# Performance work log

Hardware: AMD Instinct MI355X
Metric: run time of the kernel (lower is better)

Reference implementation:

```python
import jax, jax.numpy as jnp
import numpy as np

D_MODEL = 1024
NUM_HEADS = 16
HEAD_DIM = D_MODEL // NUM_HEADS
BATCH = 2
SEQ = 2048


def setup_inputs() -> dict:
    key = jax.random.key(0)
    ks = jax.random.split(key, 9)
    s_in = 1.0 / np.sqrt(D_MODEL)  # kaiming-ish fan-in scaling for stability
    return {
        "x": jax.random.normal(ks[0], (BATCH, SEQ, D_MODEL), jnp.float32),
        "wq": jax.random.normal(ks[1], (D_MODEL, D_MODEL), jnp.float32) * s_in,
        "bq": jnp.zeros((D_MODEL,), jnp.float32),
        "wk": jax.random.normal(ks[2], (D_MODEL, D_MODEL), jnp.float32) * s_in,
        "bk": jnp.zeros((D_MODEL,), jnp.float32),
        "wv": jax.random.normal(ks[3], (D_MODEL, D_MODEL), jnp.float32) * s_in,
        "bv": jnp.zeros((D_MODEL,), jnp.float32),
        "wo": jax.random.normal(ks[4], (D_MODEL, D_MODEL), jnp.float32) * s_in,
        "bo": jnp.zeros((D_MODEL,), jnp.float32),
    }


def reference(x, wq, bq, wk, bk, wv, bv, wo, bo):
    B, S, _ = x.shape
    # QKV projections, split heads: [B, H, S, Dh]
    def proj(w, b):
        y = x @ w + b
        return y.reshape(B, S, NUM_HEADS, HEAD_DIM).transpose(0, 2, 1, 3)

    q = proj(wq, bq)
    k = proj(wk, bk)
    v = proj(wv, bv)

    scale = 1.0 / jnp.sqrt(jnp.float32(HEAD_DIM))
    scores = jnp.einsum("bhsd,bhtd->bhst", q, k) * scale  # [B,H,S,S]
    attn = jax.nn.softmax(scores, axis=-1)
    out = jnp.einsum("bhst,bhtd->bhsd", attn, v)  # [B,H,S,Dh]
    out = out.transpose(0, 2, 1, 3).reshape(B, S, D_MODEL)
    return out @ wo + bo
```

## Files before the change

kernel.cpp:

```cpp
#include <hip/hip_runtime.h>
#include <stdint.h>
#include <stddef.h>


typedef __attribute__((ext_vector_type(8))) short short8;
typedef __attribute__((ext_vector_type(4))) float f32x4;
typedef __attribute__((ext_vector_type(16))) float f32x16;
typedef __attribute__((ext_vector_type(4))) unsigned short u16x4;

#define MFMA16(a, b, c) __builtin_amdgcn_mfma_f32_16x16x32_bf16((a), (b), (c), 0, 0, 0)
#define MFMA32(a, b, c) __builtin_amdgcn_mfma_f32_32x32x16_bf16((a), (b), (c), 0, 0, 0)
#define AS1 __attribute__((address_space(1)))
#define AS3 __attribute__((address_space(3)))

__device__ __forceinline__ unsigned short f2bf(float f) {
  union { float f; unsigned u; } v; v.f = f;
  unsigned r = v.u + 0x7fffu + ((v.u >> 16) & 1u);
  return (unsigned short)(r >> 16);
}

__device__ __forceinline__ float fexp2(float x) {
#if __has_builtin(__builtin_amdgcn_exp2f)
  return __builtin_amdgcn_exp2f(x);
#else
  return __builtin_exp2f(x);
#endif
}

__device__ __forceinline__ unsigned cvt_pk_bf16(float lo, float hi) {
  unsigned r;
  asm("v_cvt_pk_bf16_f32 %0, %1, %2" : "=v"(r) : "v"(lo), "v"(hi));
  return r;
}

__device__ __forceinline__ void pl32_swap(unsigned& a, unsigned& b) {
  asm volatile("v_permlane32_swap_b32 %0, %1" : "+v"(a), "+v"(b));
}

__device__ __forceinline__ short8 mk8(unsigned a, unsigned b, unsigned c, unsigned d) {
  union { unsigned u[4]; short8 s; } v;
  v.u[0] = a; v.u[1] = b; v.u[2] = c; v.u[3] = d;
  return v.s;
}

__global__ __launch_bounds__(256) void prep_all_kernel(const float* __restrict__ x,
                                                       const float* __restrict__ wq,
                                                       const float* __restrict__ wk,
                                                       const float* __restrict__ wv,
                                                       const float* __restrict__ wo,
                                                       const float* __restrict__ bq,
                                                       const float* __restrict__ bk,
                                                       const float* __restrict__ bv,
                                                       unsigned short* __restrict__ xb,
                                                       unsigned short* __restrict__ wt,
                                                       float* __restrict__ bias3) {
  __shared__ unsigned short t_lds[32][33];
  const int bid = blockIdx.x;
  if (bid < 4096) {
    int wsel = bid >> 10;
    int rem = bid & 1023;
    int kb = (rem >> 5) << 5;
    int nb = (rem & 31) << 5;
    const float* W = (wsel == 0) ? wq : (wsel == 1) ? wk : (wsel == 2) ? wv : wo;
    int t = threadIdx.x;
    int r = t >> 3, c = (t & 7) * 4;
    float4 v = *reinterpret_cast<const float4*>(W + (size_t)(kb + r) * 1024 + nb + c);
    t_lds[r][c + 0] = f2bf(v.x);
    t_lds[r][c + 1] = f2bf(v.y);
    t_lds[r][c + 2] = f2bf(v.z);
    t_lds[r][c + 3] = f2bf(v.w);
    __syncthreads();
    u16x4 o;
    o.x = t_lds[c + 0][r]; o.y = t_lds[c + 1][r];
    o.z = t_lds[c + 2][r]; o.w = t_lds[c + 3][r];
    *reinterpret_cast<u16x4*>(wt + (size_t)(wsel * 1024 + nb + r) * 1024 + kb + c) = o;
  } else if (bid < 8192) {
    int i = ((bid - 4096) * 256 + threadIdx.x) * 4;
    float4 v = *reinterpret_cast<const float4*>(x + i);
    u16x4 o;
    o.x = f2bf(v.x); o.y = f2bf(v.y); o.z = f2bf(v.z); o.w = f2bf(v.w);
    *reinterpret_cast<u16x4*>(xb + i) = o;
  } else {
#pragma unroll
    for (int k = 0; k < 12; ++k) {
      int i = k * 256 + threadIdx.x;
      bias3[i] = (i < 1024) ? bq[i] : (i < 2048) ? bk[i - 1024] : bv[i - 2048];
    }
  }
}

template <typename OutT, bool QS>
__global__ __launch_bounds__(256) void gemm_bt_kernel(const unsigned short* __restrict__ A,
                                                      const unsigned short* __restrict__ Bt,
                                                      const float* __restrict__ bias,
                                                      OutT* __restrict__ C, int N) {
  constexpr int K = 1024;
  __shared__ __align__(16) unsigned short a_lds[2][128 * 32];
  __shared__ __align__(16) unsigned short b_lds[2][128 * 32];
  const int nb = N >> 7;
  const int nwg = nb << 5;
  const int cpx = nwg >> 3;
  const int wg = ((int)blockIdx.x & 7) * cpx + ((int)blockIdx.x >> 3);
  const int bm = wg / nb;
  const int bn = wg % nb;
  const int m0 = bm << 7, n0 = bn << 7;
  const int tid = threadIdx.x;
  const int w = tid >> 6, l = tid & 63;
  const int lr = l & 15, lg = l >> 4;
  const int wm = (w >> 1) << 6, wn = (w & 1) << 6;

  const int q0 = w * 2, q1 = w * 2 + 1;
  const unsigned short* pa0 = A + (size_t)(m0 + q0 * 16 + (l >> 2)) * K + (l & 3) * 8;
  const unsigned short* pa1 = A + (size_t)(m0 + q1 * 16 + (l >> 2)) * K + (l & 3) * 8;
  const unsigned short* pb0 = Bt + (size_t)(n0 + q0 * 16 + (l >> 2)) * K + (l & 3) * 8;
  const unsigned short* pb1 = Bt + (size_t)(n0 + q1 * 16 + (l >> 2)) * K + (l & 3) * 8;

#define GEMM_STAGE(buf, k0)                                                        \
  do {                                                                             \
    __builtin_amdgcn_global_load_lds((const AS1 void*)(pa0 + (k0)),                \
        (AS3 void*)(&a_lds[buf][q0 * 512]), 16, 0, 0);                             \
    __builtin_amdgcn_global_load_lds((const AS1 void*)(pa1 + (k0)),                \
        (AS3 void*)(&a_lds[buf][q1 * 512]), 16, 0, 0);                             \
    __builtin_amdgcn_global_load_lds((const AS1 void*)(pb0 + (k0)),                \
        (AS3 void*)(&b_lds[buf][q0 * 512]), 16, 0, 0);                             \
    __builtin_amdgcn_global_load_lds((const AS1 void*)(pb1 + (k0)),                \
        (AS3 void*)(&b_lds[buf][q1 * 512]), 16, 0, 0);                             \
  } while (0)

  f32x4 acc[4][4] = {};
  GEMM_STAGE(0, 0);
  __syncthreads();

  int cur = 0;
  for (int k0 = 0; k0 < K; k0 += 32) {
    if (k0 + 32 < K) GEMM_STAGE(cur ^ 1, k0 + 32);
    short8 af[4], bfr[4];
#pragma unroll
    for (int i = 0; i < 4; ++i)
      af[i] = *reinterpret_cast<const short8*>(&a_lds[cur][(wm + i * 16 + lr) * 32 + lg * 8]);
#pragma unroll
    for (int i = 0; i < 4; ++i)
      bfr[i] = *reinterpret_cast<const short8*>(&b_lds[cur][(wn + i * 16 + lr) * 32 + lg * 8]);
#pragma unroll
    for (int i = 0; i < 4; ++i)
#pragma unroll
      for (int j = 0; j < 4; ++j)
        acc[i][j] = MFMA16(af[i], bfr[j], acc[i][j]);
    __syncthreads();
    cur ^= 1;
  }
#undef GEMM_STAGE

  const float scale = (QS && n0 < 1024) ? 0.18033688011111f : 1.0f;
#pragma unroll
  for (int i = 0; i < 4; ++i) {
#pragma unroll
    for (int j = 0; j < 4; ++j) {
#pragma unroll
      for (int r = 0; r < 4; ++r) {
        int m = m0 + wm + i * 16 + lg * 4 + r;
        int n = n0 + wn + j * 16 + lr;
        float val = (acc[i][j][r] + bias[n]) * scale;
        if constexpr (sizeof(OutT) == 2) {
          C[(size_t)m * N + n] = (OutT)f2bf(val);
        } else {
          C[(size_t)m * N + n] = val;
        }
      }
    }
  }
}

__device__ __forceinline__ void stage_v(char* vw, int pi, int vd0, short8 va, short8 vb) {
  union { short8 s; unsigned u[4]; } ua, ub;
  ua.s = va; ub.s = vb;
#pragma unroll
  for (int jr = 0; jr < 4; ++jr) {
    unsigned w0 = __builtin_amdgcn_perm(ub.u[jr], ua.u[jr], 0x05040100u);
    unsigned w1 = __builtin_amdgcn_perm(ub.u[jr], ua.u[jr], 0x07060302u);
    int d0 = vd0 + 2 * jr, d1 = d0 + 1;
    *reinterpret_cast<unsigned*>(vw + d0 * 128 + ((4 * pi) ^ ((d0 & 7) << 4))) = w0;
    *reinterpret_cast<unsigned*>(vw + d1 * 128 + ((4 * pi) ^ ((d1 & 7) << 4))) = w1;
  }
}

__global__ __launch_bounds__(512, 4) void attn_kernel(const unsigned short* __restrict__ qkv,
                                                       unsigned short* __restrict__ aout) {
  __shared__ __align__(16) char lds[65536];
  const int tid = threadIdx.x;
  const int w = tid >> 6, l = tid & 63;
  const int kv = w >> 2, wsub = w & 3;
  const int lq = l & 31;
  const int hi = l >> 5;
  const int wg = ((int)blockIdx.x & 7) * 64 + ((int)blockIdx.x >> 3);
  const int bh = wg >> 4, qblk = wg & 15;
  const int b = bh >> 4, h = bh & 15;
  const size_t rowbase = (size_t)b * 2048;
  const int q0 = qblk * 128 + wsub * 32;
  const int base = kv << 15;

  short8 qf[4];
  {
    const unsigned short* qrow = qkv + (rowbase + q0 + lq) * 3072 + h * 64 + hi * 8;
#pragma unroll
    for (int c = 0; c < 4; ++c)
      qf[c] = *reinterpret_cast<const short8*>(qrow + c * 16);
  }

  const int colsw = (16 * (l & 7)) ^ ((l >> 3) << 4);
  const char* ksrc = (const char*)(qkv + (rowbase + kv * 1024) * 3072 + 1024 + h * 64) +
                     (size_t)(16 * wsub + (l >> 3)) * 6144 + colsw;
  const int kdst = wsub * 2048;

  const int pi = tid & 31;
  const int vd0 = ((tid >> 5) & 7) * 8;
  const unsigned short* vbase = qkv + (rowbase + kv * 1024) * 3072 + 2048 + h * 64;
  const int swz_lq = (lq & 7) << 4;

  short8 ones;
  {
    union { unsigned u[4]; short8 s; } o_;
    o_.u[0] = o_.u[1] = o_.u[2] = o_.u[3] = 0x3F803F80u;
    ones = o_.s;
  }

  f32x16 ot0 = {}, ot1 = {}, lacc = {};

  __builtin_amdgcn_global_load_lds((const AS1 void*)ksrc,
                                   (AS3 void*)(lds + base + kdst), 16, 0, 0);
  __builtin_amdgcn_global_load_lds((const AS1 void*)(ksrc + 49152),
                                   (AS3 void*)(lds + base + kdst + 1024), 16, 0, 0);
  ksrc += 393216;
  {
    short8 va = *reinterpret_cast<const short8*>(vbase + (size_t)(2 * pi) * 3072 + vd0);
    short8 vb = *reinterpret_cast<const short8*>(vbase + (size_t)(2 * pi + 1) * 3072 + vd0);
    stage_v(lds + base + 16384, pi, vd0, va, vb);
  }

  int cur = 0;
  for (int t0 = 0; t0 < 1024; t0 += 64) {
    __syncthreads();
    const bool more = (t0 + 64) < 1024;
    short8 vna, vnb;
    if (more) {
      char* kd = lds + base + ((cur ^ 1) << 13) + kdst;
      __builtin_amdgcn_global_load_lds((const AS1 void*)ksrc, (AS3 void*)kd, 16, 0, 0);
      __builtin_amdgcn_global_load_lds((const AS1 void*)(ksrc + 49152),
                                       (AS3 void*)(kd + 1024), 16, 0, 0);
      ksrc += 393216;
      vna = *reinterpret_cast<const short8*>(vbase + (size_t)(t0 + 64 + 2 * pi) * 3072 + vd0);
      vnb = *reinterpret_cast<const short8*>(vbase + (size_t)(t0 + 65 + 2 * pi) * 3072 + vd0);
    }
    const char* kl = lds + base + (cur << 13);
    const char* vl = lds + base + 16384 + (cur << 13);

    f32x16 s0 = {}, s1 = {};
    __builtin_amdgcn_s_setprio(1);
#pragma unroll
    for (int c = 0; c < 4; ++c) {
      short8 kf0 = *reinterpret_cast<const short8*>(kl + lq * 128 + ((c * 32 + hi * 16) ^ swz_lq));
      short8 kf1 = *reinterpret_cast<const short8*>(kl + (32 + lq) * 128 + ((c * 32 + hi * 16) ^ swz_lq));
      s0 = MFMA32(kf0, qf[c], s0);
      s1 = MFMA32(kf1, qf[c], s1);
    }
    __builtin_amdgcn_s_setprio(0);

    if (more) stage_v(lds + base + 16384 + ((cur ^ 1) << 13), pi, vd0, vna, vnb);

#pragma unroll
    for (int c = 0; c < 4; ++c) {
      float t0_, t1_, t2_, t3_, t4_, t5_, t6_, t7_;
      if (c < 2) {
        const int o = c * 8;
        t0_ = fexp2(s0[o + 0]); t1_ = fexp2(s0[o + 1]);
        t2_ = fexp2(s0[o + 2]); t3_ = fexp2(s0[o + 3]);
        t4_ = fexp2(s0[o + 4]); t5_ = fexp2(s0[o + 5]);
        t6_ = fexp2(s0[o + 6]); t7_ = fexp2(s0[o + 7]);
      } else {
        const int o = (c - 2) * 8;
        t0_ = fexp2(s1[o + 0]); t1_ = fexp2(s1[o + 1]);
        t2_ = fexp2(s1[o + 2]); t3_ = fexp2(s1[o + 3]);
        t4_ = fexp2(s1[o + 4]); t5_ = fexp2(s1[o + 5]);
        t6_ = fexp2(s1[o + 6]); t7_ = fexp2(s1[o + 7]);
      }
      unsigned a0 = cvt_pk_bf16(t0_, t1_), a1 = cvt_pk_bf16(t4_, t5_);
      unsigned b0 = cvt_pk_bf16(t2_, t3_), b1 = cvt_pk_bf16(t6_, t7_);
      pl32_swap(a0, a1); pl32_swap(b0, b1);
      short8 pfc = mk8(a0, b0, a1, b1);
      short8 vf0 = *reinterpret_cast<const short8*>(vl + lq * 128 + ((c * 32 + hi * 16) ^ swz_lq));
      short8 vf1 = *reinterpret_cast<const short8*>(vl + (32 + lq) * 128 + ((c * 32 + hi * 16) ^ swz_lq));
      __builtin_amdgcn_s_setprio(1);
      ot0 = MFMA32(vf0, pfc, ot0);
      ot1 = MFMA32(vf1, pfc, ot1);
      lacc = MFMA32(ones, pfc, lacc);
      __builtin_amdgcn_s_setprio(0);
    }
    cur ^= 1;
  }

  __syncthreads();
  float* lbuf = (float*)lds;
  if (kv == 1) {
    float* ob = (float*)(lds + 32768 + wsub * 8192);
#pragma unroll
    for (int r = 0; r < 16; ++r) {
      int d = (r & 3) + 8 * (r >> 2) + 4 * hi;
      ob[d * 32 + lq] = ot0[r];
      ob[(32 + d) * 32 + lq] = ot1[r];
    }
    if (hi == 0) lbuf[wsub * 32 + lq] = lacc[0];
  }
  __syncthreads();
  if (kv == 0) {
    const float* ob = (const float*)(lds + 32768 + wsub * 8192);
    const float inv = 1.0f / (lacc[0] + lbuf[wsub * 32 + lq]);
    char* st = lds + 8192;
    const int qq = wsub * 32 + lq;
    const int swz = (qq & 7) << 4;
#pragma unroll
    for (int r = 0; r < 16; r += 2) {
      int d = (r & 3) + 8 * (r >> 2) + 4 * hi;
      float a0 = (ot0[r] + ob[d * 32 + lq]) * inv;
      float a1 = (ot0[r + 1] + ob[(d + 1) * 32 + lq]) * inv;
      *(unsigned*)(st + qq * 128 + ((2 * d) ^ swz)) = cvt_pk_bf16(a0, a1);
      float b0_ = (ot1[r] + ob[(32 + d) * 32 + lq]) * inv;
      float b1_ = (ot1[r + 1] + ob[(33 + d) * 32 + lq]) * inv;
      *(unsigned*)(st + qq * 128 + ((2 * (32 + d)) ^ swz)) = cvt_pk_bf16(b0_, b1_);
    }
  }
  __syncthreads();
  {
    int row = tid >> 2;
    int c2 = (tid & 3) * 2;
    int swzr = (row & 7) << 4;
    const char* src = lds + 8192 + row * 128;
    short8 v0 = *reinterpret_cast<const short8*>(src + ((c2 * 16) ^ swzr));
    short8 v1 = *reinterpret_cast<const short8*>(src + (((c2 + 1) * 16) ^ swzr));
    unsigned short* orow = aout + (rowbase + qblk * 128 + row) * 1024 + h * 64 + c2 * 8;
    *reinterpret_cast<short8*>(orow) = v0;
    *reinterpret_cast<short8*>(orow + 8) = v1;
  }
}

extern "C" void kernel_launch(void* const* d_in, const int* in_sizes, int n_in,
                              void* d_out, int out_size, void* d_ws, size_t ws_size,
                              hipStream_t stream) {
  const float* x  = (const float*)d_in[0];
  const float* wq = (const float*)d_in[1];
  const float* bq = (const float*)d_in[2];
  const float* wk = (const float*)d_in[3];
  const float* bk = (const float*)d_in[4];
  const float* wv = (const float*)d_in[5];
  const float* bv = (const float*)d_in[6];
  const float* wo = (const float*)d_in[7];
  const float* bo = (const float*)d_in[8];
  float* out = (float*)d_out;

  char* ws = (char*)d_ws;
  unsigned short* xb    = (unsigned short*)(ws);
  unsigned short* aob   = (unsigned short*)(ws);
  unsigned short* wt    = (unsigned short*)(ws + 8388608);
  float*          bias3 = (float*)(ws + 16777216);
  unsigned short* qkvb  = (unsigned short*)(ws + 16842752);

  prep_all_kernel<<<8193, 256, 0, stream>>>(x, wq, wk, wv, wo, bq, bk, bv, xb, wt, bias3);

  gemm_bt_kernel<unsigned short, true><<<768, 256, 0, stream>>>(xb, wt, bias3, qkvb, 3072);

  attn_kernel<<<512, 512, 0, stream>>>(qkvb, aob);

  gemm_bt_kernel<float, false><<<256, 256, 0, stream>>>(aob, wt + (size_t)3072 * 1024, bo, out, 1024);
}
```

Measured before the change: 116.0 us.

## Pre-transpose V in a separate kernel and stream it via async LDS loads

Adds a kernel that writes V in per-head transposed [d][t] layout to workspace. The attention kernel then loads V tiles with global_load_lds, the same way it loads K, instead of register loads followed by perm-based LDS staging. This drops per-iteration VGPR traffic and the perm work inside the attention loop. In exchange it adds a kernel launch and an extra round trip of V (about 8 MB) through global memory.

```diff
diff --git a/kernel.cpp b/kernel.cpp
--- a/kernel.cpp
+++ b/kernel.cpp
@@ -89,6 +89,29 @@
   }
 }
 
+__global__ __launch_bounds__(256) void vt_kernel(const unsigned short* __restrict__ qkv,
+                                                 unsigned short* __restrict__ vt) {
+  __shared__ unsigned short t_lds[32][33];
+  const int bid = blockIdx.x;
+  const int T0 = (bid >> 5) << 5;
+  const int D0 = (bid & 31) << 5;
+  const int t = threadIdx.x;
+  const int r = t >> 3, c = (t & 7) * 4;
+  u16x4 v = *reinterpret_cast<const u16x4*>(qkv + (size_t)(T0 + r) * 3072 + 2048 + D0 + c);
+  t_lds[r][c + 0] = v.x;
+  t_lds[r][c + 1] = v.y;
+  t_lds[r][c + 2] = v.z;
+  t_lds[r][c + 3] = v.w;
+  __syncthreads();
+  u16x4 o;
+  o.x = t_lds[c + 0][r]; o.y = t_lds[c + 1][r];
+  o.z = t_lds[c + 2][r]; o.w = t_lds[c + 3][r];
+  const int d = D0 + r;
+  const int b = T0 >> 11, h = d >> 6, dloc = d & 63;
+  *reinterpret_cast<u16x4*>(vt + (size_t)(b * 16 + h) * 131072 + (size_t)dloc * 2048 +
+                            (T0 & 2047) + c) = o;
+}
+
 template <typename OutT, bool QS>
 __global__ __launch_bounds__(256) void gemm_bt_kernel(const unsigned short* __restrict__ A,
                                                       const unsigned short* __restrict__ Bt,
@@ -171,21 +194,9 @@
   }
 }
 
-__device__ __forceinline__ void stage_v(char* vw, int pi, int vd0, short8 va, short8 vb) {
-  union { short8 s; unsigned u[4]; } ua, ub;
-  ua.s = va; ub.s = vb;
-#pragma unroll
-  for (int jr = 0; jr < 4; ++jr) {
-    unsigned w0 = __builtin_amdgcn_perm(ub.u[jr], ua.u[jr], 0x05040100u);
-    unsigned w1 = __builtin_amdgcn_perm(ub.u[jr], ua.u[jr], 0x07060302u);
-    int d0 = vd0 + 2 * jr, d1 = d0 + 1;
-    *reinterpret_cast<unsigned*>(vw + d0 * 128 + ((4 * pi) ^ ((d0 & 7) << 4))) = w0;
-    *reinterpret_cast<unsigned*>(vw + d1 * 128 + ((4 * pi) ^ ((d1 & 7) << 4))) = w1;
-  }
-}
-
 __global__ __launch_bounds__(512, 4) void attn_kernel(const unsigned short* __restrict__ qkv,
-                                                       unsigned short* __restrict__ aout) {
+                                                      const unsigned short* __restrict__ vt,
+                                                      unsigned short* __restrict__ aout) {
   __shared__ __align__(16) char lds[65536];
   const int tid = threadIdx.x;
   const int w = tid >> 6, l = tid & 63;
@@ -210,11 +221,10 @@
   const int colsw = (16 * (l & 7)) ^ ((l >> 3) << 4);
   const char* ksrc = (const char*)(qkv + (rowbase + kv * 1024) * 3072 + 1024 + h * 64) +
                      (size_t)(16 * wsub + (l >> 3)) * 6144 + colsw;
+  const char* vsrc = (const char*)vt + (size_t)bh * 262144 +
+                     (size_t)(16 * wsub + (l >> 3)) * 4096 + kv * 2048 + colsw;
   const int kdst = wsub * 2048;
 
-  const int pi = tid & 31;
-  const int vd0 = ((tid >> 5) & 7) * 8;
-  const unsigned short* vbase = qkv + (rowbase + kv * 1024) * 3072 + 2048 + h * 64;
   const int swz_lq = (lq & 7) << 4;
 
   short8 ones;
@@ -230,26 +240,28 @@
                                    (AS3 void*)(lds + base + kdst), 16, 0, 0);
   __builtin_amdgcn_global_load_lds((const AS1 void*)(ksrc + 49152),
                                    (AS3 void*)(lds + base + kdst + 1024), 16, 0, 0);
+  __builtin_amdgcn_global_load_lds((const AS1 void*)vsrc,
+                                   (AS3 void*)(lds + base + 16384 + kdst), 16, 0, 0);
+  __builtin_amdgcn_global_load_lds((const AS1 void*)(vsrc + 32768),
+                                   (AS3 void*)(lds + base + 16384 + kdst + 1024), 16, 0, 0);
   ksrc += 393216;
-  {
-    short8 va = *reinterpret_cast<const short8*>(vbase + (size_t)(2 * pi) * 3072 + vd0);
-    short8 vb = *reinterpret_cast<const short8*>(vbase + (size_t)(2 * pi + 1) * 3072 + vd0);
-    stage_v(lds + base + 16384, pi, vd0, va, vb);
-  }
+  vsrc += 128;
 
   int cur = 0;
   for (int t0 = 0; t0 < 1024; t0 += 64) {
     __syncthreads();
     const bool more = (t0 + 64) < 1024;
-    short8 vna, vnb;
     if (more) {
       char* kd = lds + base + ((cur ^ 1) << 13) + kdst;
       __builtin_amdgcn_global_load_lds((const AS1 void*)ksrc, (AS3 void*)kd, 16, 0, 0);
       __builtin_amdgcn_global_load_lds((const AS1 void*)(ksrc + 49152),
                                        (AS3 void*)(kd + 1024), 16, 0, 0);
+      __builtin_amdgcn_global_load_lds((const AS1 void*)vsrc,
+                                       (AS3 void*)(kd + 16384), 16, 0, 0);
+      __builtin_amdgcn_global_load_lds((const AS1 void*)(vsrc + 32768),
+                                       (AS3 void*)(kd + 16384 + 1024), 16, 0, 0);
       ksrc += 393216;
-      vna = *reinterpret_cast<const short8*>(vbase + (size_t)(t0 + 64 + 2 * pi) * 3072 + vd0);
-      vnb = *reinterpret_cast<const short8*>(vbase + (size_t)(t0 + 65 + 2 * pi) * 3072 + vd0);
+      vsrc += 128;
     }
     const char* kl = lds + base + (cur << 13);
     const char* vl = lds + base + 16384 + (cur << 13);
@@ -264,8 +276,6 @@
       s1 = MFMA32(kf1, qf[c], s1);
     }
     __builtin_amdgcn_s_setprio(0);
-
-    if (more) stage_v(lds + base + 16384 + ((cur ^ 1) << 13), pi, vd0, vna, vnb);
 
 #pragma unroll
     for (int c = 0; c < 4; ++c) {
@@ -362,12 +372,15 @@
   unsigned short* wt    = (unsigned short*)(ws + 8388608);
   float*          bias3 = (float*)(ws + 16777216);
   unsigned short* qkvb  = (unsigned short*)(ws + 16842752);
+  unsigned short* vtb   = (unsigned short*)(ws + 42008576);
 
   prep_all_kernel<<<8193, 256, 0, stream>>>(x, wq, wk, wv, wo, bq, bk, bv, xb, wt, bias3);
 
   gemm_bt_kernel<unsigned short, true><<<768, 256, 0, stream>>>(xb, wt, bias3, qkvb, 3072);
 
-  attn_kernel<<<512, 512, 0, stream>>>(qkvb, aob);
+  vt_kernel<<<4096, 256, 0, stream>>>(qkvb, vtb);
+
+  attn_kernel<<<512, 512, 0, stream>>>(qkvb, vtb, aob);
 
   gemm_bt_kernel<float, false><<<256, 256, 0, stream>>>(aob, wt + (size_t)3072 * 1024, bo, out, 1024);
 }
```

Result: no change. 117.2 us (+1.1%).
